# Optimization experiments

Hardware: AMD Instinct MI355X
Metric: run time of the kernel (lower is better)

The kernel has to match this reference:

```python
import jax, jax.numpy as jnp
import numpy as np

D_MODEL = 1024
HEADS = 16
D_K = D_MODEL // HEADS
B, S = 2, 2048
NEG = -1e9


def setup_inputs() -> dict:
    key = jax.random.key(0)
    ks = jax.random.split(key, 12)
    sc = 1.0 / np.sqrt(D_MODEL)
    inp = {
        'query': jax.random.normal(ks[0], (B, S, D_MODEL), jnp.float32),
        'key': jax.random.normal(ks[1], (B, S, D_MODEL), jnp.float32),
        'value': jax.random.normal(ks[2], (B, S, D_MODEL), jnp.float32),
        'mask': jnp.tril(jnp.ones((S, S), jnp.int32))[None, None],  # [1,1,S,S] causal
        'Wq': jax.random.normal(ks[3], (D_MODEL, D_MODEL), jnp.float32) * sc,
        'bq': jax.random.normal(ks[4], (D_MODEL,), jnp.float32) * 0.02,
        'Wk': jax.random.normal(ks[5], (D_MODEL, D_MODEL), jnp.float32) * sc,
        'bk': jax.random.normal(ks[6], (D_MODEL,), jnp.float32) * 0.02,
        'Wv': jax.random.normal(ks[7], (D_MODEL, D_MODEL), jnp.float32) * sc,
        'bv': jax.random.normal(ks[8], (D_MODEL,), jnp.float32) * 0.02,
        'Wo': jax.random.normal(ks[9], (D_MODEL, D_MODEL), jnp.float32) * sc,
        'bo': jax.random.normal(ks[10], (D_MODEL,), jnp.float32) * 0.02,
    }
    return inp


def reference(query, key, value, mask, Wq, bq, Wk, bk, Wv, bv, Wo, bo):
    # QKV projections (torch Linear: x @ W.T + b; here W stored as [in,out])
    def split_heads(x):  # [B,S,D] -> [B,H,S,dk]
        return x.reshape(B, S, HEADS, D_K).transpose(0, 2, 1, 3)

    q = split_heads(query @ Wq + bq)
    k = split_heads(key @ Wk + bk)
    v = split_heads(value @ Wv + bv)

    scores = jnp.einsum('bhqd,bhkd->bhqk', q, k) / np.sqrt(D_K)
    scores = jnp.where(mask == 0, NEG, scores)
    attn = jax.nn.softmax(scores, axis=-1)  # dropout p=0 (eval) -> identity
    out = jnp.einsum('bhqk,bhkd->bhqd', attn, v)
    out = out.transpose(0, 2, 1, 3).reshape(B, S, D_MODEL)
    return out @ Wo + bo
```

## Files before the change

### kernel.cpp

```cpp
#include <hip/hip_runtime.h>
#include <hip/hip_bf16.h>
#include <cstdint>
#include <cstddef>

typedef short short8 __attribute__((ext_vector_type(8)));
typedef float f32x4 __attribute__((ext_vector_type(4)));
typedef float f32x16 __attribute__((ext_vector_type(16)));

#define SS 2048
#define DK 64
#define LAMBDA 0.18033688011112042f

__device__ __forceinline__ float b2f(ushort u) {
    union { uint32_t i; float f; } x; x.i = ((uint32_t)u) << 16; return x.f;
}
__device__ __forceinline__ ushort f2b(float f) {
    union { float f; uint32_t i; } x; x.f = f;
    uint32_t r = (x.i + 0x7fffu + ((x.i >> 16) & 1u)) >> 16;
    return (ushort)r;
}
__device__ __forceinline__ uint32_t pk_bf16(float a, float b) {
    union { __hip_bfloat162 v; uint32_t u; } x;
    float2 f2; f2.x = a; f2.y = b;
    x.v = __float22bfloat162_rn(f2);
    return x.u;
}

__device__ __forceinline__ void gl_lds16(const ushort* __restrict__ g, ushort* l) {
    __builtin_amdgcn_global_load_lds(
        (const __attribute__((address_space(1))) uint32_t*)(uintptr_t)g,
        (__attribute__((address_space(3))) uint32_t*)(uintptr_t)l, 16, 0, 0);
}

__device__ __forceinline__ bool probe_bf16(const uint32_t* __restrict__ probe) {
    const int lane = threadIdx.x & 63;
    int c = 0;
#pragma unroll
    for (int i = 0; i < 4; ++i) {
        uint32_t u = probe[lane * 4 + i];
        uint32_t e = (u >> 7) & 0xffu;
        c += (e >= 100u && e <= 140u) ? 1 : 0;
    }
    unsigned long long b = __ballot(c >= 3);
    return __popcll(b) > 32;
}

__device__ __forceinline__ void ld8_f32_to_bf16(ushort* dst, const float* __restrict__ src) {
    float4 a = *(const float4*)src;
    float4 b = *(const float4*)(src + 4);
    ushort t[8] = {f2b(a.x), f2b(a.y), f2b(a.z), f2b(a.w),
                   f2b(b.x), f2b(b.y), f2b(b.z), f2b(b.w)};
    *(uint4*)dst = *(uint4*)t;
}

__global__ __launch_bounds__(256) void transpose_all(const void* __restrict__ W0,
                                                     const void* __restrict__ W1,
                                                     const void* __restrict__ W2,
                                                     const void* __restrict__ W3,
                                                     ushort* __restrict__ ws,
                                                     const uint32_t* __restrict__ probe,
                                                     size_t wotOff) {
    __shared__ __align__(16) ushort t[64 * 72];
    const bool isbf = probe_bf16(probe);
    const int z = blockIdx.z;
    const void* W = (z == 0) ? W0 : (z == 1) ? W1 : (z == 2) ? W2 : W3;
    ushort* T = ws + ((z < 3) ? ((size_t)z << 20) : wotOff);

    const int n0 = blockIdx.x * 64, k0 = blockIdx.y * 64;
    const int tid = threadIdx.x;
    const int r = tid >> 3, cg = (tid & 7) * 8;
    if (isbf) {
        const ushort* Wb = (const ushort*)W;
#pragma unroll
        for (int p = 0; p < 2; ++p) {
            int k = r + p * 32;
            *(uint4*)&t[k * 72 + cg] = *(const uint4*)&Wb[(size_t)(k0 + k) * 1024 + n0 + cg];
        }
    } else {
        const float* Wf = (const float*)W;
#pragma unroll
        for (int p = 0; p < 2; ++p) {
            int k = r + p * 32;
            ld8_f32_to_bf16(&t[k * 72 + cg], &Wf[(size_t)(k0 + k) * 1024 + n0 + cg]);
        }
    }
    __syncthreads();
#pragma unroll
    for (int p = 0; p < 2; ++p) {
        int n = r + p * 32;
        uint4 o;
        ushort* op = (ushort*)&o;
#pragma unroll
        for (int i = 0; i < 8; ++i) op[i] = t[(cg + i) * 72 + n];
        *(uint4*)&T[(size_t)(n0 + n) * 1024 + k0 + cg] = o;
    }
}

__global__ __launch_bounds__(256) void conv_qkv(const void* __restrict__ q,
                                                const void* __restrict__ k,
                                                const void* __restrict__ v,
                                                ushort* __restrict__ ws,
                                                const uint32_t* __restrict__ probe,
                                                size_t dstOff) {
    const bool isbf = probe_bf16(probe);
    if (isbf) return;
    const int z = blockIdx.y;
    const void* src = (z == 0) ? q : (z == 1) ? k : v;
    ushort* dst = ws + dstOff + ((size_t)z << 22);
    const size_t i = ((size_t)blockIdx.x * 256 + threadIdx.x) * 8;
    ld8_f32_to_bf16(&dst[i], &((const float*)src)[i]);
}

template <int PRE>
__global__ __launch_bounds__(256, 3) void qkv_gemm(const void* __restrict__ qp,
                                                   const void* __restrict__ kp,
                                                   const void* __restrict__ vp,
                                                   const void* __restrict__ bqp,
                                                   const void* __restrict__ bkp,
                                                   const void* __restrict__ bvp,
                                                   ushort* __restrict__ ws,
                                                   const uint32_t* __restrict__ probe) {
    __shared__ __align__(16) ushort As[3][128 * 32];
    __shared__ __align__(16) ushort Bs[3][128 * 32];
    const bool isbf = probe_bf16(probe);
    const int z = blockIdx.z;
    const ushort* Bt = ws + ((size_t)z << 20);
    const void* bias = (z == 0) ? bqp : (z == 1) ? bkp : bvp;
    ushort* C = ws + ((size_t)((PRE ? 16 : 5) + 4 * z) << 20);
    const float scl = (z == 0) ? LAMBDA : 1.0f;

    const int tid = threadIdx.x;
    const int lane = tid & 63, wid = tid >> 6;
    const int l15 = lane & 15, g = lane >> 4;
    const int wm = wid >> 1, wn = wid & 1;
    const int id0 = blockIdx.y * 8 + blockIdx.x;
    const int id = (id0 & 7) * 32 + (id0 >> 3);
    const int m0 = (id >> 3) * 128, n0 = (id & 7) * 128;
    const int sr = tid >> 2, sc = (tid & 3) * 8;
    const int lrow = (lane >> 2), lcol = (lane & 3) * 8;

    f32x4 acc[4][4];
#pragma unroll
    for (int i = 0; i < 4; ++i)
#pragma unroll
        for (int j = 0; j < 4; ++j) {
            f32x4 zz = {0.f, 0.f, 0.f, 0.f};
            acc[i][j] = zz;
        }

    if (PRE) {
        const ushort* Ab = isbf ? (const ushort*)((z == 0) ? qp : (z == 1) ? kp : vp)
                                : ws + ((size_t)(4 + 4 * z) << 20);
        auto stage1 = [&](int kk, int bsel) {
#pragma unroll
            for (int q = 0; q < 2; ++q) {
                const int row = (wid * 2 + q) * 16 + lrow;
                gl_lds16(&Bt[(size_t)(n0 + row) * 1024 + kk + lcol],
                         &Bs[bsel][(wid * 2 + q) * 512]);
                gl_lds16(&Ab[(size_t)(m0 + row) * 1024 + kk + lcol],
                         &As[bsel][(wid * 2 + q) * 512]);
            }
        };
        stage1(0, 0);
        stage1(32, 1);
        asm volatile("s_waitcnt vmcnt(4)" ::: "memory");
        __builtin_amdgcn_s_barrier();
        __builtin_amdgcn_sched_barrier(0);
        int cur = 0;
#pragma unroll 1
        for (int kk = 0; kk < 1024; kk += 32) {
            const int nxt = (cur >= 1) ? cur - 1 : cur + 2;
            if (kk + 64 < 1024) stage1(kk + 64, nxt);
            short8 a[4], b[4];
#pragma unroll
            for (int i = 0; i < 4; ++i)
                a[i] = *(const short8*)&As[cur][(wm * 64 + i * 16 + l15) * 32 + g * 8];
#pragma unroll
            for (int j = 0; j < 4; ++j)
                b[j] = *(const short8*)&Bs[cur][(wn * 64 + j * 16 + l15) * 32 + g * 8];
#pragma unroll
            for (int i = 0; i < 4; ++i)
#pragma unroll
                for (int j = 0; j < 4; ++j)
                    acc[i][j] =
                        __builtin_amdgcn_mfma_f32_16x16x32_bf16(a[i], b[j], acc[i][j], 0, 0, 0);
            if (kk + 32 < 1024) {
                if (kk + 64 < 1024)
                    asm volatile("s_waitcnt vmcnt(4)" ::: "memory");
                else
                    asm volatile("s_waitcnt vmcnt(0)" ::: "memory");
                __builtin_amdgcn_s_barrier();
                __builtin_amdgcn_sched_barrier(0);
            }
            cur = (cur == 2) ? 0 : cur + 1;
        }
    } else {
        auto stageAB = [&](int kk, int bsel) {
#pragma unroll
            for (int q = 0; q < 2; ++q) {
                const int row = (wid * 2 + q) * 16 + lrow;
                gl_lds16(&Bt[(size_t)(n0 + row) * 1024 + kk + lcol],
                         &Bs[bsel][(wid * 2 + q) * 512]);
            }
            const void* A = (z == 0) ? qp : (z == 1) ? kp : vp;
            if (isbf) {
                const ushort* Ab = (const ushort*)A;
#pragma unroll
                for (int q = 0; q < 2; ++q) {
                    const int row = (wid * 2 + q) * 16 + lrow;
                    gl_lds16(&Ab[(size_t)(m0 + row) * 1024 + kk + lcol],
                             &As[bsel][(wid * 2 + q) * 512]);
                }
            } else {
                const float* Af = (const float*)A;
                ld8_f32_to_bf16(&As[bsel][sr * 32 + sc], &Af[(size_t)(m0 + sr) * 1024 + kk + sc]);
                ld8_f32_to_bf16(&As[bsel][(sr + 64) * 32 + sc],
                                &Af[(size_t)(m0 + sr + 64) * 1024 + kk + sc]);
            }
        };
        stageAB(0, 0);
        __syncthreads();
#pragma unroll 2
        for (int kk = 0; kk < 1024; kk += 32) {
            const int cur = (kk >> 5) & 1;
            if (kk < 1024 - 32) stageAB(kk + 32, cur ^ 1);
            short8 a[4], b[4];
#pragma unroll
            for (int i = 0; i < 4; ++i)
                a[i] = *(const short8*)&As[cur][(wm * 64 + i * 16 + l15) * 32 + g * 8];
#pragma unroll
            for (int j = 0; j < 4; ++j)
                b[j] = *(const short8*)&Bs[cur][(wn * 64 + j * 16 + l15) * 32 + g * 8];
#pragma unroll
            for (int i = 0; i < 4; ++i)
#pragma unroll
                for (int j = 0; j < 4; ++j)
                    acc[i][j] =
                        __builtin_amdgcn_mfma_f32_16x16x32_bf16(a[i], b[j], acc[i][j], 0, 0, 0);
            __syncthreads();
        }
    }

#pragma unroll
    for (int i = 0; i < 4; ++i)
#pragma unroll
        for (int j = 0; j < 4; ++j) {
            const int col = n0 + wn * 64 + j * 16 + l15;
            const float bv = isbf ? b2f(((const ushort*)bias)[col]) : ((const float*)bias)[col];
#pragma unroll
            for (int r = 0; r < 4; ++r) {
                const int row = m0 + wm * 64 + i * 16 + g * 4 + r;
                const float v = (acc[i][j][r] + bv) * scl;
                size_t idx;
                if (z != 2) {
                    idx = ((size_t)((row >> 11) * 16 + (col >> 6)) * SS + (row & 2047)) * 64 +
                          (col & 63);
                } else {
                    idx = ((size_t)((row >> 11) * 16 + (col >> 6)) * 64 + (col & 63)) * SS +
                          (row & 2047);
                }
                C[idx] = f2b(v);
            }
        }
}

__global__ __launch_bounds__(256) void out_gemm(const ushort* __restrict__ A,
                                                const ushort* __restrict__ Bt,
                                                const void* __restrict__ bias,
                                                void* __restrict__ C,
                                                const uint32_t* __restrict__ probe) {
    __shared__ __align__(16) ushort As[3][64 * 32];
    __shared__ __align__(16) ushort Bs[3][128 * 32];
    const bool isbf = probe_bf16(probe);
    const int tid = threadIdx.x;
    const int lane = tid & 63, wid = tid >> 6;
    const int l15 = lane & 15, g = lane >> 4;
    const int wm = wid >> 1, wn = wid & 1;
    const int id0 = blockIdx.y * 8 + blockIdx.x;
    const int id = (id0 & 7) * 64 + (id0 >> 3);
    const int m0 = (id >> 3) * 64, n0 = (id & 7) * 128;
    const int lrow = (lane >> 2), lcol = (lane & 3) * 8;

    f32x4 acc[2][4];
#pragma unroll
    for (int i = 0; i < 2; ++i)
#pragma unroll
        for (int j = 0; j < 4; ++j) {
            f32x4 zz = {0.f, 0.f, 0.f, 0.f};
            acc[i][j] = zz;
        }

    auto stage1 = [&](int kk, int bsel) {
        {
            const int row = wid * 16 + lrow;
            gl_lds16(&A[(size_t)(m0 + row) * 1024 + kk + lcol], &As[bsel][wid * 512]);
        }
#pragma unroll
        for (int q = 0; q < 2; ++q) {
            const int row = (wid * 2 + q) * 16 + lrow;
            gl_lds16(&Bt[(size_t)(n0 + row) * 1024 + kk + lcol], &Bs[bsel][(wid * 2 + q) * 512]);
        }
    };

    stage1(0, 0);
    stage1(32, 1);
    asm volatile("s_waitcnt vmcnt(3)" ::: "memory");
    __builtin_amdgcn_s_barrier();
    __builtin_amdgcn_sched_barrier(0);
    int cur = 0;
#pragma unroll 1
    for (int kk = 0; kk < 1024; kk += 32) {
        const int nxt = (cur >= 1) ? cur - 1 : cur + 2;
        if (kk + 64 < 1024) stage1(kk + 64, nxt);
        short8 a[2], b[4];
#pragma unroll
        for (int i = 0; i < 2; ++i)
            a[i] = *(const short8*)&As[cur][(wm * 32 + i * 16 + l15) * 32 + g * 8];
#pragma unroll
        for (int j = 0; j < 4; ++j)
            b[j] = *(const short8*)&Bs[cur][(wn * 64 + j * 16 + l15) * 32 + g * 8];
#pragma unroll
        for (int i = 0; i < 2; ++i)
#pragma unroll
            for (int j = 0; j < 4; ++j)
                acc[i][j] = __builtin_amdgcn_mfma_f32_16x16x32_bf16(a[i], b[j], acc[i][j], 0, 0, 0);
        if (kk + 32 < 1024) {
            if (kk + 64 < 1024)
                asm volatile("s_waitcnt vmcnt(3)" ::: "memory");
            else
                asm volatile("s_waitcnt vmcnt(0)" ::: "memory");
            __builtin_amdgcn_s_barrier();
            __builtin_amdgcn_sched_barrier(0);
        }
        cur = (cur == 2) ? 0 : cur + 1;
    }

#pragma unroll
    for (int i = 0; i < 2; ++i)
#pragma unroll
        for (int j = 0; j < 4; ++j) {
            const int col = n0 + wn * 64 + j * 16 + l15;
            const float bv = isbf ? b2f(((const ushort*)bias)[col]) : ((const float*)bias)[col];
#pragma unroll
            for (int r = 0; r < 4; ++r) {
                const int row = m0 + wm * 32 + i * 16 + g * 4 + r;
                const float v = acc[i][j][r] + bv;
                const size_t idx = (size_t)row * 1024 + col;
                if (isbf)
                    ((ushort*)C)[idx] = f2b(v);
                else
                    ((float*)C)[idx] = v;
            }
        }
}

__global__ __launch_bounds__(256, 2) void attn_fwd(const ushort* __restrict__ Q,
                                                   const ushort* __restrict__ K,
                                                   const ushort* __restrict__ Vt,
                                                   ushort* __restrict__ O) {
    __shared__ __align__(16) ushort Ks[3][8 * 512];
    __shared__ __align__(16) ushort Vs[3][8 * 512];

    const int y = blockIdx.y;
    const int s0i = (blockIdx.x + y) & 15;
    const int t = (y & 16) ? (15 - s0i) : s0i;
    const int tid = threadIdx.x;
    const int lane = tid & 63, wid = tid >> 6;
    const int l31 = lane & 31, h = lane >> 5;

    const ushort* Qb = Q + (size_t)y * SS * DK;
    const ushort* Kb = K + (size_t)y * SS * DK;
    const ushort* Vb = Vt + (size_t)y * DK * SS;
    const int b = y >> 4, hh = y & 15;

    const int q0w = t * 128 + wid * 32;
    const int nkt = 2 * t + 2;

    short8 qf[4];
#pragma unroll
    for (int k4 = 0; k4 < 4; ++k4)
        qf[k4] = *(const short8*)&Qb[(size_t)(q0w + l31) * 64 + k4 * 16 + h * 8];

    const int f0 = wid * 2, f1 = f0 + 1;
    const ushort* kb0 = Kb + (size_t)((f0 >> 2) * 32 + l31) * 64 + (f0 & 3) * 16 + h * 8;
    const ushort* kb1 = Kb + (size_t)((f1 >> 2) * 32 + l31) * 64 + (f1 & 3) * 16 + h * 8;
    const ushort* vb0 = Vb + (size_t)((f0 >> 2) * 32 + l31) * SS + (f0 & 3) * 16 + h * 8;
    const ushort* vb1 = Vb + (size_t)((f1 >> 2) * 32 + l31) * SS + (f1 & 3) * 16 + h * 8;

    const int lo8 = lane * 8;

    f32x16 acc[2];
#pragma unroll
    for (int nt = 0; nt < 2; ++nt)
#pragma unroll
        for (int r = 0; r < 16; ++r) acc[nt][r] = 0.f;
    float lpA = 0.f, lpB = 0.f;

    auto stageKV = [&](int kt, int bsel) {
        const size_t ko = (size_t)kt * 4096;
        const int vo = kt * 64;
        gl_lds16(kb0 + ko, &Ks[bsel][f0 * 512]);
        gl_lds16(kb1 + ko, &Ks[bsel][f1 * 512]);
        gl_lds16(vb0 + vo, &Vs[bsel][f0 * 512]);
        gl_lds16(vb1 + vo, &Vs[bsel][f1 * 512]);
    };

    stageKV(0, 0);
    stageKV(1, 1);
    asm volatile("s_waitcnt vmcnt(4)" ::: "memory");
    __builtin_amdgcn_s_barrier();
    __builtin_amdgcn_sched_barrier(0);

    int cur = 0;
#pragma unroll 1
    for (int kt = 0; kt < nkt; ++kt) {
        if (kt + 2 < nkt) {
            const int nxt = (cur >= 1) ? cur - 1 : cur + 2;
            stageKV(kt + 2, nxt);
        }

        if (q0w + 31 >= kt * 64) {
            f32x16 sc[2];
#pragma unroll
            for (int st = 0; st < 2; ++st)
#pragma unroll
                for (int r = 0; r < 16; ++r) sc[st][r] = 0.f;
#pragma unroll
            for (int st = 0; st < 2; ++st)
#pragma unroll
                for (int k4 = 0; k4 < 4; ++k4) {
                    short8 kb = *(const short8*)&Ks[cur][(st * 4 + k4) * 512 + lo8];
                    sc[st] = __builtin_amdgcn_mfma_f32_32x32x16_bf16(kb, qf[k4], sc[st], 0, 0, 0);
                }

            if (kt >= nkt - 2) {
                const int qg = q0w + l31;
#pragma unroll
                for (int st = 0; st < 2; ++st)
#pragma unroll
                    for (int r = 0; r < 16; ++r) {
                        const int kvg = kt * 64 + st * 32 + (r & 3) + 8 * (r >> 2) + 4 * h;
                        if (kvg > qg) sc[st][r] = -1e9f;
                    }
            }

            uint32_t pk8[2][8];
#pragma unroll
            for (int st = 0; st < 2; ++st) {
                float ls = 0.f;
#pragma unroll
                for (int i = 0; i < 8; ++i) {
                    const float p0 = exp2f(sc[st][2 * i]);
                    const float p1 = exp2f(sc[st][2 * i + 1]);
                    ls += p0 + p1;
                    pk8[st][i] = pk_bf16(p0, p1);
                }
                if (st == 0) lpA += ls; else lpB += ls;
            }

#pragma unroll
            for (int st = 0; st < 2; ++st) {
                asm("v_permlane32_swap_b32 %0, %1" : "+v"(pk8[st][0]), "+v"(pk8[st][2]));
                asm("v_permlane32_swap_b32 %0, %1" : "+v"(pk8[st][1]), "+v"(pk8[st][3]));
                asm("v_permlane32_swap_b32 %0, %1" : "+v"(pk8[st][4]), "+v"(pk8[st][6]));
                asm("v_permlane32_swap_b32 %0, %1" : "+v"(pk8[st][5]), "+v"(pk8[st][7]));
            }

#pragma unroll
            for (int ktv = 0; ktv < 4; ++ktv) {
                union { uint32_t u[4]; short8 s; } pa;
#pragma unroll
                for (int w4 = 0; w4 < 4; ++w4) pa.u[w4] = pk8[ktv >> 1][(ktv & 1) * 4 + w4];
#pragma unroll
                for (int nt = 0; nt < 2; ++nt) {
                    short8 vb = *(const short8*)&Vs[cur][(nt * 4 + ktv) * 512 + lo8];
                    acc[nt] =
                        __builtin_amdgcn_mfma_f32_32x32x16_bf16(pa.s, vb, acc[nt], 0, 0, 0);
                }
            }
        }

        if (kt + 1 < nkt) {
            if (kt + 2 < nkt)
                asm volatile("s_waitcnt vmcnt(4)" ::: "memory");
            else
                asm volatile("s_waitcnt vmcnt(0)" ::: "memory");
            __builtin_amdgcn_s_barrier();
            __builtin_amdgcn_sched_barrier(0);
        }
        cur = (cur == 2) ? 0 : cur + 1;
    }

    const float lp = lpA + lpB;
    const float lt = lp + __shfl_xor(lp, 32);
    const float inv = 1.0f / lt;
#pragma unroll
    for (int r = 0; r < 16; ++r) {
        const int qrow = (r & 3) + 8 * (r >> 2) + 4 * h;
        const float ivr = __shfl(inv, qrow);
        const int rowg = q0w + qrow;
#pragma unroll
        for (int nt = 0; nt < 2; ++nt) {
            const int col = hh * 64 + nt * 32 + l31;
            O[(size_t)(b * SS + rowg) * 1024 + col] = f2b(acc[nt][r] * ivr);
        }
    }
}

extern "C" void kernel_launch(void* const* d_in, const int* in_sizes, int n_in,
                              void* d_out, int out_size, void* d_ws, size_t ws_size,
                              hipStream_t stream) {
    const void* q = d_in[0];
    const void* k = d_in[1];
    const void* v = d_in[2];
    const void* Wq = d_in[4];
    const void* bq = d_in[5];
    const void* Wk = d_in[6];
    const void* bk = d_in[7];
    const void* Wv = d_in[8];
    const void* bv = d_in[9];
    const void* Wo = d_in[10];
    const void* bo = d_in[11];
    const uint32_t* probe = (const uint32_t*)d_in[0];

    ushort* ws = (ushort*)d_ws;
    const size_t M = (size_t)1 << 20;
    const bool pre = ws_size >= 28 * M * sizeof(ushort);

    if (pre) {
        transpose_all<<<dim3(16, 16, 4), 256, 0, stream>>>(Wq, Wk, Wv, Wo, ws, probe, 3 * M);
        conv_qkv<<<dim3(2048, 3), 256, 0, stream>>>(q, k, v, ws, probe, 4 * M);
        qkv_gemm<1><<<dim3(8, 32, 3), 256, 0, stream>>>(q, k, v, bq, bk, bv, ws, probe);
        attn_fwd<<<dim3(16, 32), 256, 0, stream>>>(ws + 16 * M, ws + 20 * M, ws + 24 * M,
                                                   ws + 4 * M);
        out_gemm<<<dim3(8, 64), 256, 0, stream>>>(ws + 4 * M, ws + 3 * M, bo, d_out, probe);
    } else {
        transpose_all<<<dim3(16, 16, 4), 256, 0, stream>>>(Wq, Wk, Wv, Wo, ws, probe, 4 * M);
        qkv_gemm<0><<<dim3(8, 32, 3), 256, 0, stream>>>(q, k, v, bq, bk, bv, ws, probe);
        attn_fwd<<<dim3(16, 32), 256, 0, stream>>>(ws + 5 * M, ws + 9 * M, ws + 13 * M, ws);
        out_gemm<<<dim3(8, 64), 256, 0, stream>>>(ws, ws + 4 * M, bo, d_out, probe);
    }
}
```

Measured before the change: 234.7 us.

## Software-pipeline QK^T one tile ahead with 4-stage KV ring and setprio

Grows the K/V LDS ring from 3 to 4 stages and prefetches three tiles ahead. It also computes the QK^T MFMAs for tile kt+1 before the softmax and PV of tile kt, so matrix work overlaps the exp and permute ALU work. The softmax+PV section is wrapped in s_setprio(1). This adds LDS usage and registers for the extra score accumulator, which may reduce occupancy under launch_bounds(256,2). The waitcnt and barrier logic was changed, so a sync race is possible.

After: 238.3 us. No clear change (+1.6%).

```diff
diff --git a/kernel.cpp b/kernel.cpp
--- a/kernel.cpp
+++ b/kernel.cpp
@@ -358,8 +358,8 @@
                                                    const ushort* __restrict__ K,
                                                    const ushort* __restrict__ Vt,
                                                    ushort* __restrict__ O) {
-    __shared__ __align__(16) ushort Ks[3][8 * 512];
-    __shared__ __align__(16) ushort Vs[3][8 * 512];
+    __shared__ __align__(16) ushort Ks[4][8 * 512];
+    __shared__ __align__(16) ushort Vs[4][8 * 512];
 
     const int y = blockIdx.y;
     const int s0i = (blockIdx.x + y) & 15;
@@ -396,7 +396,8 @@
         for (int r = 0; r < 16; ++r) acc[nt][r] = 0.f;
     float lpA = 0.f, lpB = 0.f;
 
-    auto stageKV = [&](int kt, int bsel) {
+    auto stageKV = [&](int kt) {
+        const int bsel = kt & 3;
         const size_t ko = (size_t)kt * 4096;
         const int vo = kt * 64;
         gl_lds16(kb0 + ko, &Ks[bsel][f0 * 512]);
@@ -405,34 +406,48 @@
         gl_lds16(vb1 + vo, &Vs[bsel][f1 * 512]);
     };
 
-    stageKV(0, 0);
-    stageKV(1, 1);
-    asm volatile("s_waitcnt vmcnt(4)" ::: "memory");
+    auto qk = [&](int kt, f32x16* sc) {
+        const int bsel = kt & 3;
+#pragma unroll
+        for (int st = 0; st < 2; ++st) {
+#pragma unroll
+            for (int r = 0; r < 16; ++r) sc[st][r] = 0.f;
+#pragma unroll
+            for (int k4 = 0; k4 < 4; ++k4) {
+                short8 kb = *(const short8*)&Ks[bsel][(st * 4 + k4) * 512 + lo8];
+                sc[st] = __builtin_amdgcn_mfma_f32_32x32x16_bf16(kb, qf[k4], sc[st], 0, 0, 0);
+            }
+        }
+    };
+
+    stageKV(0);
+    stageKV(1);
+    if (nkt > 2) {
+        stageKV(2);
+        asm volatile("s_waitcnt vmcnt(4)" ::: "memory");
+    } else {
+        asm volatile("s_waitcnt vmcnt(0)" ::: "memory");
+    }
     __builtin_amdgcn_s_barrier();
     __builtin_amdgcn_sched_barrier(0);
 
-    int cur = 0;
+    f32x16 scn[2];
+    qk(0, scn);
+
 #pragma unroll 1
     for (int kt = 0; kt < nkt; ++kt) {
-        if (kt + 2 < nkt) {
-            const int nxt = (cur >= 1) ? cur - 1 : cur + 2;
-            stageKV(kt + 2, nxt);
-        }
-
-        if (q0w + 31 >= kt * 64) {
-            f32x16 sc[2];
-#pragma unroll
-            for (int st = 0; st < 2; ++st)
-#pragma unroll
-                for (int r = 0; r < 16; ++r) sc[st][r] = 0.f;
-#pragma unroll
-            for (int st = 0; st < 2; ++st)
-#pragma unroll
-                for (int k4 = 0; k4 < 4; ++k4) {
-                    short8 kb = *(const short8*)&Ks[cur][(st * 4 + k4) * 512 + lo8];
-                    sc[st] = __builtin_amdgcn_mfma_f32_32x32x16_bf16(kb, qf[k4], sc[st], 0, 0, 0);
-                }
-
+        if (kt + 3 < nkt) stageKV(kt + 3);
+
+        const bool live = (q0w + 31 >= kt * 64);
+
+        f32x16 sc[2];
+#pragma unroll
+        for (int st = 0; st < 2; ++st) sc[st] = scn[st];
+
+        __builtin_amdgcn_s_setprio(1);
+        if (kt + 1 < nkt && q0w + 31 >= (kt + 1) * 64) qk(kt + 1, scn);
+
+        if (live) {
             if (kt >= nkt - 2) {
                 const int qg = q0w + l31;
 #pragma unroll
@@ -466,6 +481,7 @@
                 asm("v_permlane32_swap_b32 %0, %1" : "+v"(pk8[st][5]), "+v"(pk8[st][7]));
             }
 
+            const int vsel = kt & 3;
 #pragma unroll
             for (int ktv = 0; ktv < 4; ++ktv) {
                 union { uint32_t u[4]; short8 s; } pa;
@@ -473,22 +489,22 @@
                 for (int w4 = 0; w4 < 4; ++w4) pa.u[w4] = pk8[ktv >> 1][(ktv & 1) * 4 + w4];
 #pragma unroll
                 for (int nt = 0; nt < 2; ++nt) {
-                    short8 vb = *(const short8*)&Vs[cur][(nt * 4 + ktv) * 512 + lo8];
+                    short8 vb = *(const short8*)&Vs[vsel][(nt * 4 + ktv) * 512 + lo8];
                     acc[nt] =
                         __builtin_amdgcn_mfma_f32_32x32x16_bf16(pa.s, vb, acc[nt], 0, 0, 0);
                 }
             }
         }
+        __builtin_amdgcn_s_setprio(0);
 
         if (kt + 1 < nkt) {
-            if (kt + 2 < nkt)
+            if (kt + 3 < nkt)
                 asm volatile("s_waitcnt vmcnt(4)" ::: "memory");
-            else
+            else if (kt + 2 < nkt)
                 asm volatile("s_waitcnt vmcnt(0)" ::: "memory");
             __builtin_amdgcn_s_barrier();
             __builtin_amdgcn_sched_barrier(0);
         }
-        cur = (cur == 2) ? 0 : cur + 1;
     }
 
     const float lp = lpA + lpB;
```
